# Kernel tuning notes

Hardware: AMD Instinct MI355X
Metric: run time of the kernel (lower is better)

The kernel has to match this reference:

```python
import jax, jax.numpy as jnp
import numpy as np

B = 65536      # batch
S = 256        # state_dim
A = 8          # n_agents
NA = 16        # n_actions
K = 10         # num_kernel
H = 64         # adv_hypernet_embed
AD = A * NA    # action_dim
D = S + AD     # state_dim + action_dim


def setup_inputs() -> dict:
    key = jax.random.key(0)
    ks = jax.random.split(key, 20)
    sc = 0.05
    inp = {
        'states': jax.random.normal(ks[0], (B, S), jnp.float32),
        'actions_onehot': jax.random.uniform(ks[1], (B, A, NA), jnp.float32),
        # key extractors: S -> H -> H -> 1, stacked over K kernels
        'kW1': jax.random.normal(ks[2], (K, H, S), jnp.float32) * sc,
        'kb1': jnp.zeros((K, H), jnp.float32),
        'kW2': jax.random.normal(ks[3], (K, H, H), jnp.float32) * sc,
        'kb2': jnp.zeros((K, H), jnp.float32),
        'kW3': jax.random.normal(ks[4], (K, 1, H), jnp.float32) * sc,
        'kb3': jnp.zeros((K, 1), jnp.float32),
        # agents extractors: S -> H -> H -> A
        'aW1': jax.random.normal(ks[5], (K, H, S), jnp.float32) * sc,
        'ab1': jnp.zeros((K, H), jnp.float32),
        'aW2': jax.random.normal(ks[6], (K, H, H), jnp.float32) * sc,
        'ab2': jnp.zeros((K, H), jnp.float32),
        'aW3': jax.random.normal(ks[7], (K, A, H), jnp.float32) * sc,
        'ab3': jnp.zeros((K, A), jnp.float32),
        # action extractors: S+AD -> H -> H -> A
        'cW1': jax.random.normal(ks[8], (K, H, D), jnp.float32) * sc,
        'cb1': jnp.zeros((K, H), jnp.float32),
        'cW2': jax.random.normal(ks[9], (K, H, H), jnp.float32) * sc,
        'cb2': jnp.zeros((K, H), jnp.float32),
        'cW3': jax.random.normal(ks[10], (K, A, H), jnp.float32) * sc,
        'cb3': jnp.zeros((K, A), jnp.float32),
    }
    return inp


def _mlp3(x, W1, b1, W2, b2, W3, b3):
    # x: [B, in] ; W1: [K, H, in] -> batched over K kernels in one GEMM
    h = jax.nn.relu(jnp.einsum('bd,khd->bkh', x, W1) + b1)        # [B,K,H]
    h = jax.nn.relu(jnp.einsum('bkh,kgh->bkg', h, W2) + b2)       # [B,K,H]
    return jnp.einsum('bkh,koh->bko', h, W3) + b3                 # [B,K,out]


def reference(states, actions_onehot,
              kW1, kb1, kW2, kb2, kW3, kb3,
              aW1, ab1, aW2, ab2, aW3, ab3,
              cW1, cb1, cW2, cb2, cW3, cb3):
    actions_flat = actions_onehot.reshape(states.shape[0], -1)    # [B, A*NA]
    data = jnp.concatenate([states, actions_flat], axis=1)        # [B, S+AD]

    x_key = jnp.abs(_mlp3(states, kW1, kb1, kW2, kb2, kW3, kb3)) + 1e-10   # [B,K,1]
    x_agents = jax.nn.sigmoid(_mlp3(states, aW1, ab1, aW2, ab2, aW3, ab3)) # [B,K,A]
    x_action = jax.nn.sigmoid(_mlp3(data, cW1, cb1, cW2, cb2, cW3, cb3))   # [B,K,A]

    # broadcast key over agents, multiply gates, sum over the K kernels
    head_attend = jnp.sum(x_key * x_agents * x_action, axis=1)    # [B,A]
    return head_attend
```

## Files before the change

### kernel.cpp

```cpp
#include <hip/hip_runtime.h>
#include <hip/hip_bf16.h>

#define Bsz 65536
#define Sdim 256
#define Aag 8
#define Kk 10
#define ADdim 128

#define SLAB_K_ELEMS 72704
#define NET_ELEMS 21504

typedef float f32x4 __attribute__((ext_vector_type(4)));
typedef __bf16 bf16x8 __attribute__((ext_vector_type(8)));

#define MFMA(a, b, cacc) __builtin_amdgcn_mfma_f32_16x16x32_bf16((a), (b), (cacc), 0, 0, 0)

__device__ __forceinline__ __bf16 f2bf(float f) {
    return (__bf16)f;
}

__device__ __forceinline__ unsigned int pack_bf2(float a, float b) {
    union { unsigned short s[2]; unsigned int u; } cv;
    union { unsigned short s; __bf16 b; } x;
    x.b = f2bf(a); cv.s[0] = x.s;
    x.b = f2bf(b); cv.s[1] = x.s;
    return cv.u;
}

__device__ __forceinline__ bf16x8 cvt8(float4 lo, float4 hi) {
    bf16x8 v;
    v[0] = f2bf(lo.x); v[1] = f2bf(lo.y); v[2] = f2bf(lo.z); v[3] = f2bf(lo.w);
    v[4] = f2bf(hi.x); v[5] = f2bf(hi.y); v[6] = f2bf(hi.z); v[7] = f2bf(hi.w);
    return v;
}

__device__ __forceinline__ int gperm(int n) {
    return ((n >> 5) << 5) + (((n >> 2) & 3) << 3) + (((n >> 4) & 1) << 2) + (n & 3);
}

__global__ void prep_weights(const float* __restrict__ kW1, const float* __restrict__ aW1,
                             const float* __restrict__ cW1, const float* __restrict__ kW2,
                             const float* __restrict__ aW2, const float* __restrict__ cW2,
                             const float* __restrict__ kW3, const float* __restrict__ aW3,
                             const float* __restrict__ cW3, __bf16* __restrict__ out) {
    int gid = blockIdx.x * 256 + threadIdx.x;
    if (gid >= 90880) return;
    int k = gid / 9088;
    int r = gid - k * 9088;
    int t, cn;
    if (r < 2688)      { t = 0; cn = r; }
    else if (r < 5376) { t = 1; cn = r - 2688; }
    else               { t = 2; cn = r - 5376; }
    const int KN = (t == 2) ? 384 : 256;
    const int CPR = KN / 8;
    const float* W1 = (t == 0) ? kW1 : (t == 1) ? aW1 : cW1;
    const float* W2 = (t == 0) ? kW2 : (t == 1) ? aW2 : cW2;
    const float* W3 = (t == 0) ? kW3 : (t == 1) ? aW3 : cW3;
    const int rows3 = (t == 0) ? 1 : 8;
    int dstchunk;
    const float* src = nullptr;
    if (cn < 64 * CPR) {
        int n = cn / CPR, k8 = cn - n * CPR;
        src = W1 + ((size_t)(k * 64 + gperm(n))) * KN + k8 * 8;
        dstchunk = n * CPR + (k8 ^ (n & 7));
    } else if (cn < 64 * CPR + 512) {
        int c2 = cn - 64 * CPR;
        int n = c2 >> 3, k8 = c2 & 7;
        src = W2 + ((size_t)(k * 64 + gperm(n))) * 64 + k8 * 8;
        dstchunk = 64 * CPR + n * 8 + (k8 ^ (n & 7));
    } else {
        int c3 = cn - 64 * CPR - 512;
        int n = c3 >> 3, k8 = c3 & 7;
        if (n < rows3) src = W3 + ((size_t)(k * rows3 + n)) * 64 + k8 * 8;
        dstchunk = 64 * CPR + 512 + n * 8 + (k8 ^ (n & 7));
    }
    bf16x8 v;
#pragma unroll
    for (int e = 0; e < 8; ++e) v[e] = src ? f2bf(src[e]) : (__bf16)0.0f;
    *(bf16x8*)(out + (size_t)k * SLAB_K_ELEMS + t * NET_ELEMS + dstchunk * 8) = v;
}

__device__ __forceinline__ void stage(const __bf16* __restrict__ src, __bf16* dst,
                                      int nchunks, int wave, int lane) {
    const char* g = (const char*)src + lane * 16;
    for (int ci = wave; ci < nchunks; ci += 8) {
        __builtin_amdgcn_global_load_lds(
            (const __attribute__((address_space(1))) void*)(g + ci * 1024),
            (__attribute__((address_space(3))) void*)((char*)dst + ci * 1024), 16, 0, 0);
    }
}

__device__ __forceinline__ bf16x8 frag_from_hp(const unsigned int (&hp)[4][2], int kb) {
    int4 u = {(int)hp[kb * 2][0], (int)hp[kb * 2][1], (int)hp[kb * 2 + 1][0], (int)hp[kb * 2 + 1][1]};
    return __builtin_bit_cast(bf16x8, u);
}

template <int KB, int MODE>
__device__ __forceinline__ void compute_net(
    const __bf16* __restrict__ W, const bf16x8 (&xf)[2][8],
    const float* __restrict__ actions, int rowbase,
    int q, int c, int k,
    const float* __restrict__ b1p, const float* __restrict__ b2p, const float* __restrict__ b3p,
    float (&keyv)[2], float (&ag)[2][4], float (&outacc)[2][4]) {
    constexpr int CPR = KB * 4;
    constexpr int W2O = 64 * CPR * 8;
    constexpr int W3O = W2O + 4096;

    bf16x8 xa[2][4];
    if (MODE == 2) {
#pragma unroll
        for (int s = 0; s < 2; ++s) {
            const float* ap = actions + (size_t)(rowbase + s * 16 + c) * ADdim + q * 8;
#pragma unroll
            for (int kb = 0; kb < 4; ++kb)
                xa[s][kb] = cvt8(*(const float4*)(ap + kb * 32), *(const float4*)(ap + kb * 32 + 4));
        }
    }

    f32x4 acc[4][2];
#pragma unroll
    for (int mt = 0; mt < 4; ++mt) {
        int base = ((mt >> 1) << 5) + (q << 3) + ((mt & 1) << 2);
        float4 bv = *(const float4*)(b1p + k * 64 + base);
        f32x4 b = {bv.x, bv.y, bv.z, bv.w};
        acc[mt][0] = b; acc[mt][1] = b;
    }
#pragma unroll
    for (int kb = 0; kb < KB; ++kb) {
        bf16x8 b0 = (kb < 8) ? xf[0][kb] : xa[0][kb - 8];
        bf16x8 b1 = (kb < 8) ? xf[1][kb] : xa[1][kb - 8];
#pragma unroll
        for (int mt = 0; mt < 4; ++mt) {
            int n = mt * 16 + c;
            bf16x8 a = *(const bf16x8*)(W + ((n * CPR + ((kb * 4 + q) ^ (n & 7))) << 3));
            acc[mt][0] = MFMA(a, b0, acc[mt][0]);
            acc[mt][1] = MFMA(a, b1, acc[mt][1]);
        }
    }
    unsigned int hp[2][4][2];
#pragma unroll
    for (int s = 0; s < 2; ++s)
#pragma unroll
        for (int mt = 0; mt < 4; ++mt) {
            hp[s][mt][0] = pack_bf2(fmaxf(acc[mt][s][0], 0.f), fmaxf(acc[mt][s][1], 0.f));
            hp[s][mt][1] = pack_bf2(fmaxf(acc[mt][s][2], 0.f), fmaxf(acc[mt][s][3], 0.f));
        }

    f32x4 acc2[4][2];
#pragma unroll
    for (int mt = 0; mt < 4; ++mt) {
        int base = ((mt >> 1) << 5) + (q << 3) + ((mt & 1) << 2);
        float4 bv = *(const float4*)(b2p + k * 64 + base);
        f32x4 b = {bv.x, bv.y, bv.z, bv.w};
        acc2[mt][0] = b; acc2[mt][1] = b;
    }
#pragma unroll
    for (int kb = 0; kb < 2; ++kb) {
        bf16x8 bh0 = frag_from_hp(hp[0], kb);
        bf16x8 bh1 = frag_from_hp(hp[1], kb);
#pragma unroll
        for (int mt = 0; mt < 4; ++mt) {
            int n = mt * 16 + c;
            bf16x8 a2 = *(const bf16x8*)(W + W2O + ((n * 8 + ((kb * 4 + q) ^ (n & 7))) << 3));
            acc2[mt][0] = MFMA(a2, bh0, acc2[mt][0]);
            acc2[mt][1] = MFMA(a2, bh1, acc2[mt][1]);
        }
    }
#pragma unroll
    for (int s = 0; s < 2; ++s)
#pragma unroll
        for (int mt = 0; mt < 4; ++mt) {
            hp[s][mt][0] = pack_bf2(fmaxf(acc2[mt][s][0], 0.f), fmaxf(acc2[mt][s][1], 0.f));
            hp[s][mt][1] = pack_bf2(fmaxf(acc2[mt][s][2], 0.f), fmaxf(acc2[mt][s][3], 0.f));
        }

    f32x4 acc3[2];
    if (MODE == 0) {
        float b3 = b3p[k];
        f32x4 z = {0.f, 0.f, 0.f, 0.f};
        if (q == 0) z[0] = b3;
        acc3[0] = z; acc3[1] = z;
    } else {
        f32x4 z = {0.f, 0.f, 0.f, 0.f};
        if (q < 2) {
            float4 bv = *(const float4*)(b3p + k * 8 + q * 4);
            z = {bv.x, bv.y, bv.z, bv.w};
        }
        acc3[0] = z; acc3[1] = z;
    }
#pragma unroll
    for (int kb = 0; kb < 2; ++kb) {
        bf16x8 a3 = *(const bf16x8*)(W + W3O + ((c * 8 + ((kb * 4 + q) ^ (c & 7))) << 3));
#pragma unroll
        for (int s = 0; s < 2; ++s) acc3[s] = MFMA(a3, frag_from_hp(hp[s], kb), acc3[s]);
    }
#pragma unroll
    for (int s = 0; s < 2; ++s) {
        if (MODE == 0) {
            float v = __shfl(acc3[s][0], c, 64);
            keyv[s] = fabsf(v) + 1e-10f;
        } else if (MODE == 1) {
#pragma unroll
            for (int i = 0; i < 4; ++i) ag[s][i] = 1.f / (1.f + __expf(-acc3[s][i]));
        } else {
#pragma unroll
            for (int i = 0; i < 4; ++i)
                outacc[s][i] += keyv[s] * ag[s][i] * (1.f / (1.f + __expf(-acc3[s][i])));
        }
    }
}

__global__ __launch_bounds__(512, 2) void qplex_main(
    const float* __restrict__ states, const float* __restrict__ actions,
    const __bf16* __restrict__ wbf,
    const float* __restrict__ b1k, const float* __restrict__ b2k, const float* __restrict__ b3k,
    const float* __restrict__ b1a, const float* __restrict__ b2a, const float* __restrict__ b3a,
    const float* __restrict__ b1c, const float* __restrict__ b2c, const float* __restrict__ b3c,
    float* __restrict__ out) {
    __shared__ __bf16 WB[2][29696];

    const int tid = threadIdx.x;
    const int lane = tid & 63;
    const int wave = tid >> 6;
    const int q = lane >> 4;
    const int c = lane & 15;
    const int rowbase = blockIdx.x * 256 + wave * 32;

    stage(wbf, WB[0], 42, wave, lane);

    bf16x8 xf[2][8];
#pragma unroll
    for (int s = 0; s < 2; ++s) {
        const float* srow = states + (size_t)(rowbase + s * 16 + c) * Sdim + q * 8;
#pragma unroll
        for (int kb = 0; kb < 8; ++kb)
            xf[s][kb] = cvt8(*(const float4*)(srow + kb * 32), *(const float4*)(srow + kb * 32 + 4));
    }

    float keyv[2];
    float ag[2][4];
    float outacc[2][4];
#pragma unroll
    for (int s = 0; s < 2; ++s) {
        keyv[s] = 0.f;
#pragma unroll
        for (int i = 0; i < 4; ++i) { ag[s][i] = 0.f; outacc[s][i] = 0.f; }
    }

    __syncthreads();

    for (int k = 0; k < Kk; ++k) {
        const __bf16* kslab = wbf + (size_t)k * SLAB_K_ELEMS;
        stage(kslab + NET_ELEMS, WB[(k + 1) & 1], 42, wave, lane);
        compute_net<8, 0>(&WB[k & 1][0], xf, actions, rowbase, q, c, k,
                          b1k, b2k, b3k, keyv, ag, outacc);
        __syncthreads();
        stage(kslab + 2 * NET_ELEMS, WB[k & 1], 58, wave, lane);
        compute_net<8, 1>(&WB[(k + 1) & 1][0], xf, actions, rowbase, q, c, k,
                          b1a, b2a, b3a, keyv, ag, outacc);
        __syncthreads();
        if (k < Kk - 1) stage(kslab + SLAB_K_ELEMS, WB[(k + 1) & 1], 42, wave, lane);
        compute_net<12, 2>(&WB[k & 1][0], xf, actions, rowbase, q, c, k,
                           b1c, b2c, b3c, keyv, ag, outacc);
        __syncthreads();
    }

    if (q < 2) {
#pragma unroll
        for (int s = 0; s < 2; ++s) {
            int r = rowbase + s * 16 + c;
            float4 v = {outacc[s][0], outacc[s][1], outacc[s][2], outacc[s][3]};
            *(float4*)(out + (size_t)r * Aag + q * 4) = v;
        }
    }
}

extern "C" void kernel_launch(void* const* d_in, const int* in_sizes, int n_in,
                              void* d_out, int out_size, void* d_ws, size_t ws_size,
                              hipStream_t stream) {
    const float* states = (const float*)d_in[0];
    const float* actions = (const float*)d_in[1];
    const float* kW1 = (const float*)d_in[2];
    const float* kb1 = (const float*)d_in[3];
    const float* kW2 = (const float*)d_in[4];
    const float* kb2 = (const float*)d_in[5];
    const float* kW3 = (const float*)d_in[6];
    const float* kb3 = (const float*)d_in[7];
    const float* aW1 = (const float*)d_in[8];
    const float* ab1 = (const float*)d_in[9];
    const float* aW2 = (const float*)d_in[10];
    const float* ab2 = (const float*)d_in[11];
    const float* aW3 = (const float*)d_in[12];
    const float* ab3 = (const float*)d_in[13];
    const float* cW1 = (const float*)d_in[14];
    const float* cb1 = (const float*)d_in[15];
    const float* cW2 = (const float*)d_in[16];
    const float* cb2 = (const float*)d_in[17];
    const float* cW3 = (const float*)d_in[18];
    const float* cb3 = (const float*)d_in[19];
    float* out = (float*)d_out;
    __bf16* wbf = (__bf16*)d_ws;

    prep_weights<<<355, 256, 0, stream>>>(kW1, aW1, cW1, kW2, aW2, cW2, kW3, aW3, cW3, wbf);
    qplex_main<<<256, 512, 0, stream>>>(states, actions, wbf, kb1, kb2, kb3,
                                        ab1, ab2, ab3, cb1, cb2, cb3, out);
}
```

Before: 278.7 us.

## Fuse key and agent MLPs per kernel and restage weights in two regions

The key and agents networks now run together in one fused pass. Both read the same state fragments, so their MFMA chains interleave and give more independent work per wave. Shared memory is restructured from two double-buffered net slots into one per-k slab: region A holds the key and agent weights and region B holds the action weights. This cuts the barriers per k-iteration from three to two. The cost is higher register pressure from the doubled accumulators and larger staging bursts per phase.

```diff
diff --git a/kernel.cpp b/kernel.cpp
--- a/kernel.cpp
+++ b/kernel.cpp
@@ -95,26 +95,141 @@
     return __builtin_bit_cast(bf16x8, u);
 }
 
-template <int KB, int MODE>
-__device__ __forceinline__ void compute_net(
+__device__ __forceinline__ void compute_fusedKA(
+    const __bf16* __restrict__ W, const bf16x8 (&xf)[2][8],
+    int q, int c, int k,
+    const float* __restrict__ b1k, const float* __restrict__ b2k, const float* __restrict__ b3k,
+    const float* __restrict__ b1a, const float* __restrict__ b2a, const float* __restrict__ b3a,
+    float (&keyv)[2], float (&ag)[2][4]) {
+    constexpr int CPR = 32;
+    constexpr int W2O = 64 * CPR * 8;
+    constexpr int W3O = W2O + 4096;
+    const __bf16* Wa = W + NET_ELEMS;
+
+    f32x4 accK[4][2], accA[4][2];
+#pragma unroll
+    for (int mt = 0; mt < 4; ++mt) {
+        int base = ((mt >> 1) << 5) + (q << 3) + ((mt & 1) << 2);
+        float4 bk = *(const float4*)(b1k + k * 64 + base);
+        float4 ba = *(const float4*)(b1a + k * 64 + base);
+        accK[mt][0] = {bk.x, bk.y, bk.z, bk.w}; accK[mt][1] = accK[mt][0];
+        accA[mt][0] = {ba.x, ba.y, ba.z, ba.w}; accA[mt][1] = accA[mt][0];
+    }
+#pragma unroll
+    for (int kb = 0; kb < 8; ++kb) {
+        bf16x8 b0 = xf[0][kb];
+        bf16x8 b1 = xf[1][kb];
+#pragma unroll
+        for (int mt = 0; mt < 4; ++mt) {
+            int n = mt * 16 + c;
+            int off = (n * CPR + ((kb * 4 + q) ^ (n & 7))) << 3;
+            bf16x8 aK = *(const bf16x8*)(W + off);
+            bf16x8 aA = *(const bf16x8*)(Wa + off);
+            accK[mt][0] = MFMA(aK, b0, accK[mt][0]);
+            accK[mt][1] = MFMA(aK, b1, accK[mt][1]);
+            accA[mt][0] = MFMA(aA, b0, accA[mt][0]);
+            accA[mt][1] = MFMA(aA, b1, accA[mt][1]);
+        }
+    }
+    unsigned int hpK[2][4][2], hpA[2][4][2];
+#pragma unroll
+    for (int s = 0; s < 2; ++s)
+#pragma unroll
+        for (int mt = 0; mt < 4; ++mt) {
+            hpK[s][mt][0] = pack_bf2(fmaxf(accK[mt][s][0], 0.f), fmaxf(accK[mt][s][1], 0.f));
+            hpK[s][mt][1] = pack_bf2(fmaxf(accK[mt][s][2], 0.f), fmaxf(accK[mt][s][3], 0.f));
+            hpA[s][mt][0] = pack_bf2(fmaxf(accA[mt][s][0], 0.f), fmaxf(accA[mt][s][1], 0.f));
+            hpA[s][mt][1] = pack_bf2(fmaxf(accA[mt][s][2], 0.f), fmaxf(accA[mt][s][3], 0.f));
+        }
+
+    f32x4 acc2K[4][2], acc2A[4][2];
+#pragma unroll
+    for (int mt = 0; mt < 4; ++mt) {
+        int base = ((mt >> 1) << 5) + (q << 3) + ((mt & 1) << 2);
+        float4 bk = *(const float4*)(b2k + k * 64 + base);
+        float4 ba = *(const float4*)(b2a + k * 64 + base);
+        acc2K[mt][0] = {bk.x, bk.y, bk.z, bk.w}; acc2K[mt][1] = acc2K[mt][0];
+        acc2A[mt][0] = {ba.x, ba.y, ba.z, ba.w}; acc2A[mt][1] = acc2A[mt][0];
+    }
+#pragma unroll
+    for (int kb = 0; kb < 2; ++kb) {
+        bf16x8 bhK0 = frag_from_hp(hpK[0], kb);
+        bf16x8 bhK1 = frag_from_hp(hpK[1], kb);
+        bf16x8 bhA0 = frag_from_hp(hpA[0], kb);
+        bf16x8 bhA1 = frag_from_hp(hpA[1], kb);
+#pragma unroll
+        for (int mt = 0; mt < 4; ++mt) {
+            int n = mt * 16 + c;
+            int off2 = W2O + ((n * 8 + ((kb * 4 + q) ^ (n & 7))) << 3);
+            bf16x8 a2K = *(const bf16x8*)(W + off2);
+            bf16x8 a2A = *(const bf16x8*)(Wa + off2);
+            acc2K[mt][0] = MFMA(a2K, bhK0, acc2K[mt][0]);
+            acc2K[mt][1] = MFMA(a2K, bhK1, acc2K[mt][1]);
+            acc2A[mt][0] = MFMA(a2A, bhA0, acc2A[mt][0]);
+            acc2A[mt][1] = MFMA(a2A, bhA1, acc2A[mt][1]);
+        }
+    }
+#pragma unroll
+    for (int s = 0; s < 2; ++s)
+#pragma unroll
+        for (int mt = 0; mt < 4; ++mt) {
+            hpK[s][mt][0] = pack_bf2(fmaxf(acc2K[mt][s][0], 0.f), fmaxf(acc2K[mt][s][1], 0.f));
+            hpK[s][mt][1] = pack_bf2(fmaxf(acc2K[mt][s][2], 0.f), fmaxf(acc2K[mt][s][3], 0.f));
+            hpA[s][mt][0] = pack_bf2(fmaxf(acc2A[mt][s][0], 0.f), fmaxf(acc2A[mt][s][1], 0.f));
+            hpA[s][mt][1] = pack_bf2(fmaxf(acc2A[mt][s][2], 0.f), fmaxf(acc2A[mt][s][3], 0.f));
+        }
+
+    f32x4 accK3[2], accA3[2];
+    {
+        float b3 = b3k[k];
+        f32x4 zk = {0.f, 0.f, 0.f, 0.f};
+        if (q == 0) zk[0] = b3;
+        accK3[0] = zk; accK3[1] = zk;
+        f32x4 za = {0.f, 0.f, 0.f, 0.f};
+        if (q < 2) {
+            float4 bv = *(const float4*)(b3a + k * 8 + q * 4);
+            za = {bv.x, bv.y, bv.z, bv.w};
+        }
+        accA3[0] = za; accA3[1] = za;
+    }
+#pragma unroll
+    for (int kb = 0; kb < 2; ++kb) {
+        int off3 = W3O + ((c * 8 + ((kb * 4 + q) ^ (c & 7))) << 3);
+        bf16x8 a3K = *(const bf16x8*)(W + off3);
+        bf16x8 a3A = *(const bf16x8*)(Wa + off3);
+#pragma unroll
+        for (int s = 0; s < 2; ++s) {
+            accK3[s] = MFMA(a3K, frag_from_hp(hpK[s], kb), accK3[s]);
+            accA3[s] = MFMA(a3A, frag_from_hp(hpA[s], kb), accA3[s]);
+        }
+    }
+#pragma unroll
+    for (int s = 0; s < 2; ++s) {
+        float v = __shfl(accK3[s][0], c, 64);
+        keyv[s] = fabsf(v) + 1e-10f;
+#pragma unroll
+        for (int i = 0; i < 4; ++i) ag[s][i] = 1.f / (1.f + __expf(-accA3[s][i]));
+    }
+}
+
+__device__ __forceinline__ void compute_action(
     const __bf16* __restrict__ W, const bf16x8 (&xf)[2][8],
     const float* __restrict__ actions, int rowbase,
     int q, int c, int k,
     const float* __restrict__ b1p, const float* __restrict__ b2p, const float* __restrict__ b3p,
-    float (&keyv)[2], float (&ag)[2][4], float (&outacc)[2][4]) {
+    const float (&keyv)[2], const float (&ag)[2][4], float (&outacc)[2][4]) {
+    constexpr int KB = 12;
     constexpr int CPR = KB * 4;
     constexpr int W2O = 64 * CPR * 8;
     constexpr int W3O = W2O + 4096;
 
     bf16x8 xa[2][4];
-    if (MODE == 2) {
-#pragma unroll
-        for (int s = 0; s < 2; ++s) {
-            const float* ap = actions + (size_t)(rowbase + s * 16 + c) * ADdim + q * 8;
-#pragma unroll
-            for (int kb = 0; kb < 4; ++kb)
-                xa[s][kb] = cvt8(*(const float4*)(ap + kb * 32), *(const float4*)(ap + kb * 32 + 4));
-        }
+#pragma unroll
+    for (int s = 0; s < 2; ++s) {
+        const float* ap = actions + (size_t)(rowbase + s * 16 + c) * ADdim + q * 8;
+#pragma unroll
+        for (int kb = 0; kb < 4; ++kb)
+            xa[s][kb] = cvt8(*(const float4*)(ap + kb * 32), *(const float4*)(ap + kb * 32 + 4));
     }
 
     f32x4 acc[4][2];
@@ -122,8 +237,7 @@
     for (int mt = 0; mt < 4; ++mt) {
         int base = ((mt >> 1) << 5) + (q << 3) + ((mt & 1) << 2);
         float4 bv = *(const float4*)(b1p + k * 64 + base);
-        f32x4 b = {bv.x, bv.y, bv.z, bv.w};
-        acc[mt][0] = b; acc[mt][1] = b;
+        acc[mt][0] = {bv.x, bv.y, bv.z, bv.w}; acc[mt][1] = acc[mt][0];
     }
 #pragma unroll
     for (int kb = 0; kb < KB; ++kb) {
@@ -151,8 +265,7 @@
     for (int mt = 0; mt < 4; ++mt) {
         int base = ((mt >> 1) << 5) + (q << 3) + ((mt & 1) << 2);
         float4 bv = *(const float4*)(b2p + k * 64 + base);
-        f32x4 b = {bv.x, bv.y, bv.z, bv.w};
-        acc2[mt][0] = b; acc2[mt][1] = b;
+        acc2[mt][0] = {bv.x, bv.y, bv.z, bv.w}; acc2[mt][1] = acc2[mt][0];
     }
 #pragma unroll
     for (int kb = 0; kb < 2; ++kb) {
@@ -175,12 +288,7 @@
         }
 
     f32x4 acc3[2];
-    if (MODE == 0) {
-        float b3 = b3p[k];
-        f32x4 z = {0.f, 0.f, 0.f, 0.f};
-        if (q == 0) z[0] = b3;
-        acc3[0] = z; acc3[1] = z;
-    } else {
+    {
         f32x4 z = {0.f, 0.f, 0.f, 0.f};
         if (q < 2) {
             float4 bv = *(const float4*)(b3p + k * 8 + q * 4);
@@ -195,19 +303,10 @@
         for (int s = 0; s < 2; ++s) acc3[s] = MFMA(a3, frag_from_hp(hp[s], kb), acc3[s]);
     }
 #pragma unroll
-    for (int s = 0; s < 2; ++s) {
-        if (MODE == 0) {
-            float v = __shfl(acc3[s][0], c, 64);
-            keyv[s] = fabsf(v) + 1e-10f;
-        } else if (MODE == 1) {
-#pragma unroll
-            for (int i = 0; i < 4; ++i) ag[s][i] = 1.f / (1.f + __expf(-acc3[s][i]));
-        } else {
-#pragma unroll
-            for (int i = 0; i < 4; ++i)
-                outacc[s][i] += keyv[s] * ag[s][i] * (1.f / (1.f + __expf(-acc3[s][i])));
-        }
-    }
+    for (int s = 0; s < 2; ++s)
+#pragma unroll
+        for (int i = 0; i < 4; ++i)
+            outacc[s][i] += keyv[s] * ag[s][i] * (1.f / (1.f + __expf(-acc3[s][i])));
 }
 
 __global__ __launch_bounds__(512, 2) void qplex_main(
@@ -217,7 +316,9 @@
     const float* __restrict__ b1a, const float* __restrict__ b2a, const float* __restrict__ b3a,
     const float* __restrict__ b1c, const float* __restrict__ b2c, const float* __restrict__ b3c,
     float* __restrict__ out) {
-    __shared__ __bf16 WB[2][29696];
+    __shared__ __bf16 WB[SLAB_K_ELEMS];
+    __bf16* RA = WB;
+    __bf16* RB = WB + 2 * NET_ELEMS;
 
     const int tid = threadIdx.x;
     const int lane = tid & 63;
@@ -226,7 +327,7 @@
     const int c = lane & 15;
     const int rowbase = blockIdx.x * 256 + wave * 32;
 
-    stage(wbf, WB[0], 42, wave, lane);
+    stage(wbf, RA, 84, wave, lane);
 
     bf16x8 xf[2][8];
 #pragma unroll
@@ -251,17 +352,11 @@
 
     for (int k = 0; k < Kk; ++k) {
         const __bf16* kslab = wbf + (size_t)k * SLAB_K_ELEMS;
-        stage(kslab + NET_ELEMS, WB[(k + 1) & 1], 42, wave, lane);
-        compute_net<8, 0>(&WB[k & 1][0], xf, actions, rowbase, q, c, k,
-                          b1k, b2k, b3k, keyv, ag, outacc);
+        stage(kslab + 2 * NET_ELEMS, RB, 58, wave, lane);
+        compute_fusedKA(RA, xf, q, c, k, b1k, b2k, b3k, b1a, b2a, b3a, keyv, ag);
         __syncthreads();
-        stage(kslab + 2 * NET_ELEMS, WB[k & 1], 58, wave, lane);
-        compute_net<8, 1>(&WB[(k + 1) & 1][0], xf, actions, rowbase, q, c, k,
-                          b1a, b2a, b3a, keyv, ag, outacc);
-        __syncthreads();
-        if (k < Kk - 1) stage(kslab + SLAB_K_ELEMS, WB[(k + 1) & 1], 42, wave, lane);
-        compute_net<12, 2>(&WB[k & 1][0], xf, actions, rowbase, q, c, k,
-                           b1c, b2c, b3c, keyv, ag, outacc);
+        if (k < Kk - 1) stage(kslab + SLAB_K_ELEMS, RA, 84, wave, lane);
+        compute_action(RB, xf, actions, rowbase, q, c, k, b1c, b2c, b3c, keyv, ag, outacc);
         __syncthreads();
     }
 
```

After: 390.1 us. 40.0% more time.

## Read MFMA weight fragments directly from global memory instead of staging through LDS

Applied to the files above, without the earlier changes.

Removes the double-buffered LDS staging of the per-kernel weight slabs and the block-wide barriers. Each lane now loads its bf16 weight fragments straight from the global workspace, relying on L1/L2 caching. To make those loads coalesced, the prep layout becomes k8-major. Each wave now handles 16 rows instead of 32, launched as 1024 blocks of 256 threads, which trades weight reuse per load for fewer registers and higher occupancy.

```diff
diff --git a/kernel.cpp b/kernel.cpp
--- a/kernel.cpp
+++ b/kernel.cpp
@@ -62,32 +62,22 @@
     if (cn < 64 * CPR) {
         int n = cn / CPR, k8 = cn - n * CPR;
         src = W1 + ((size_t)(k * 64 + gperm(n))) * KN + k8 * 8;
-        dstchunk = n * CPR + (k8 ^ (n & 7));
+        dstchunk = k8 * 64 + n;
     } else if (cn < 64 * CPR + 512) {
         int c2 = cn - 64 * CPR;
         int n = c2 >> 3, k8 = c2 & 7;
         src = W2 + ((size_t)(k * 64 + gperm(n))) * 64 + k8 * 8;
-        dstchunk = 64 * CPR + n * 8 + (k8 ^ (n & 7));
+        dstchunk = 64 * CPR + k8 * 64 + n;
     } else {
         int c3 = cn - 64 * CPR - 512;
         int n = c3 >> 3, k8 = c3 & 7;
         if (n < rows3) src = W3 + ((size_t)(k * rows3 + n)) * 64 + k8 * 8;
-        dstchunk = 64 * CPR + 512 + n * 8 + (k8 ^ (n & 7));
+        dstchunk = 64 * CPR + 512 + k8 * 16 + n;
     }
     bf16x8 v;
 #pragma unroll
     for (int e = 0; e < 8; ++e) v[e] = src ? f2bf(src[e]) : (__bf16)0.0f;
     *(bf16x8*)(out + (size_t)k * SLAB_K_ELEMS + t * NET_ELEMS + dstchunk * 8) = v;
-}
-
-__device__ __forceinline__ void stage(const __bf16* __restrict__ src, __bf16* dst,
-                                      int nchunks, int wave, int lane) {
-    const char* g = (const char*)src + lane * 16;
-    for (int ci = wave; ci < nchunks; ci += 8) {
-        __builtin_amdgcn_global_load_lds(
-            (const __attribute__((address_space(1))) void*)(g + ci * 1024),
-            (__attribute__((address_space(3))) void*)((char*)dst + ci * 1024), 16, 0, 0);
-    }
 }
 
 __device__ __forceinline__ bf16x8 frag_from_hp(const unsigned int (&hp)[4][2], int kb) {
@@ -97,181 +87,135 @@
 
 template <int KB, int MODE>
 __device__ __forceinline__ void compute_net(
-    const __bf16* __restrict__ W, const bf16x8 (&xf)[2][8],
-    const float* __restrict__ actions, int rowbase,
+    const __bf16* __restrict__ W, const bf16x8 (&xf)[8], const bf16x8 (&xa)[4],
     int q, int c, int k,
     const float* __restrict__ b1p, const float* __restrict__ b2p, const float* __restrict__ b3p,
-    float (&keyv)[2], float (&ag)[2][4], float (&outacc)[2][4]) {
+    float& keyv, float (&ag)[4], float (&outacc)[4]) {
     constexpr int CPR = KB * 4;
     constexpr int W2O = 64 * CPR * 8;
     constexpr int W3O = W2O + 4096;
 
-    bf16x8 xa[2][4];
-    if (MODE == 2) {
-#pragma unroll
-        for (int s = 0; s < 2; ++s) {
-            const float* ap = actions + (size_t)(rowbase + s * 16 + c) * ADdim + q * 8;
-#pragma unroll
-            for (int kb = 0; kb < 4; ++kb)
-                xa[s][kb] = cvt8(*(const float4*)(ap + kb * 32), *(const float4*)(ap + kb * 32 + 4));
-        }
-    }
-
-    f32x4 acc[4][2];
+    f32x4 acc[4];
 #pragma unroll
     for (int mt = 0; mt < 4; ++mt) {
         int base = ((mt >> 1) << 5) + (q << 3) + ((mt & 1) << 2);
         float4 bv = *(const float4*)(b1p + k * 64 + base);
-        f32x4 b = {bv.x, bv.y, bv.z, bv.w};
-        acc[mt][0] = b; acc[mt][1] = b;
+        acc[mt] = {bv.x, bv.y, bv.z, bv.w};
     }
 #pragma unroll
     for (int kb = 0; kb < KB; ++kb) {
-        bf16x8 b0 = (kb < 8) ? xf[0][kb] : xa[0][kb - 8];
-        bf16x8 b1 = (kb < 8) ? xf[1][kb] : xa[1][kb - 8];
+        bf16x8 b = (kb < 8) ? xf[kb] : xa[kb - 8];
 #pragma unroll
         for (int mt = 0; mt < 4; ++mt) {
-            int n = mt * 16 + c;
-            bf16x8 a = *(const bf16x8*)(W + ((n * CPR + ((kb * 4 + q) ^ (n & 7))) << 3));
-            acc[mt][0] = MFMA(a, b0, acc[mt][0]);
-            acc[mt][1] = MFMA(a, b1, acc[mt][1]);
+            bf16x8 a = *(const bf16x8*)(W + ((kb * 256 + q * 64 + mt * 16 + c) << 3));
+            acc[mt] = MFMA(a, b, acc[mt]);
         }
     }
-    unsigned int hp[2][4][2];
-#pragma unroll
-    for (int s = 0; s < 2; ++s)
-#pragma unroll
-        for (int mt = 0; mt < 4; ++mt) {
-            hp[s][mt][0] = pack_bf2(fmaxf(acc[mt][s][0], 0.f), fmaxf(acc[mt][s][1], 0.f));
-            hp[s][mt][1] = pack_bf2(fmaxf(acc[mt][s][2], 0.f), fmaxf(acc[mt][s][3], 0.f));
-        }
-
-    f32x4 acc2[4][2];
+    unsigned int hp[4][2];
+#pragma unroll
+    for (int mt = 0; mt < 4; ++mt) {
+        hp[mt][0] = pack_bf2(fmaxf(acc[mt][0], 0.f), fmaxf(acc[mt][1], 0.f));
+        hp[mt][1] = pack_bf2(fmaxf(acc[mt][2], 0.f), fmaxf(acc[mt][3], 0.f));
+    }
+
+    f32x4 acc2[4];
 #pragma unroll
     for (int mt = 0; mt < 4; ++mt) {
         int base = ((mt >> 1) << 5) + (q << 3) + ((mt & 1) << 2);
         float4 bv = *(const float4*)(b2p + k * 64 + base);
-        f32x4 b = {bv.x, bv.y, bv.z, bv.w};
-        acc2[mt][0] = b; acc2[mt][1] = b;
+        acc2[mt] = {bv.x, bv.y, bv.z, bv.w};
     }
 #pragma unroll
     for (int kb = 0; kb < 2; ++kb) {
-        bf16x8 bh0 = frag_from_hp(hp[0], kb);
-        bf16x8 bh1 = frag_from_hp(hp[1], kb);
+        bf16x8 bh = frag_from_hp(hp, kb);
 #pragma unroll
         for (int mt = 0; mt < 4; ++mt) {
-            int n = mt * 16 + c;
-            bf16x8 a2 = *(const bf16x8*)(W + W2O + ((n * 8 + ((kb * 4 + q) ^ (n & 7))) << 3));
-            acc2[mt][0] = MFMA(a2, bh0, acc2[mt][0]);
-            acc2[mt][1] = MFMA(a2, bh1, acc2[mt][1]);
+            bf16x8 a2 = *(const bf16x8*)(W + W2O + ((kb * 256 + q * 64 + mt * 16 + c) << 3));
+            acc2[mt] = MFMA(a2, bh, acc2[mt]);
         }
     }
 #pragma unroll
-    for (int s = 0; s < 2; ++s)
-#pragma unroll
-        for (int mt = 0; mt < 4; ++mt) {
-            hp[s][mt][0] = pack_bf2(fmaxf(acc2[mt][s][0], 0.f), fmaxf(acc2[mt][s][1], 0.f));
-            hp[s][mt][1] = pack_bf2(fmaxf(acc2[mt][s][2], 0.f), fmaxf(acc2[mt][s][3], 0.f));
-        }
-
-    f32x4 acc3[2];
+    for (int mt = 0; mt < 4; ++mt) {
+        hp[mt][0] = pack_bf2(fmaxf(acc2[mt][0], 0.f), fmaxf(acc2[mt][1], 0.f));
+        hp[mt][1] = pack_bf2(fmaxf(acc2[mt][2], 0.f), fmaxf(acc2[mt][3], 0.f));
+    }
+
+    f32x4 acc3;
     if (MODE == 0) {
         float b3 = b3p[k];
         f32x4 z = {0.f, 0.f, 0.f, 0.f};
         if (q == 0) z[0] = b3;
-        acc3[0] = z; acc3[1] = z;
+        acc3 = z;
     } else {
         f32x4 z = {0.f, 0.f, 0.f, 0.f};
         if (q < 2) {
             float4 bv = *(const float4*)(b3p + k * 8 + q * 4);
             z = {bv.x, bv.y, bv.z, bv.w};
         }
-        acc3[0] = z; acc3[1] = z;
+        acc3 = z;
     }
 #pragma unroll
     for (int kb = 0; kb < 2; ++kb) {
-        bf16x8 a3 = *(const bf16x8*)(W + W3O + ((c * 8 + ((kb * 4 + q) ^ (c & 7))) << 3));
-#pragma unroll
-        for (int s = 0; s < 2; ++s) acc3[s] = MFMA(a3, frag_from_hp(hp[s], kb), acc3[s]);
-    }
-#pragma unroll
-    for (int s = 0; s < 2; ++s) {
-        if (MODE == 0) {
-            float v = __shfl(acc3[s][0], c, 64);
-            keyv[s] = fabsf(v) + 1e-10f;
-        } else if (MODE == 1) {
-#pragma unroll
-            for (int i = 0; i < 4; ++i) ag[s][i] = 1.f / (1.f + __expf(-acc3[s][i]));
-        } else {
-#pragma unroll
-            for (int i = 0; i < 4; ++i)
-                outacc[s][i] += keyv[s] * ag[s][i] * (1.f / (1.f + __expf(-acc3[s][i])));
-        }
-    }
-}
-
-__global__ __launch_bounds__(512, 2) void qplex_main(
+        bf16x8 a3 = *(const bf16x8*)(W + W3O + ((kb * 64 + q * 16 + c) << 3));
+        acc3 = MFMA(a3, frag_from_hp(hp, kb), acc3);
+    }
+    if (MODE == 0) {
+        float v = __shfl(acc3[0], c, 64);
+        keyv = fabsf(v) + 1e-10f;
+    } else if (MODE == 1) {
+#pragma unroll
+        for (int i = 0; i < 4; ++i) ag[i] = 1.f / (1.f + __expf(-acc3[i]));
+    } else {
+#pragma unroll
+        for (int i = 0; i < 4; ++i)
+            outacc[i] += keyv * ag[i] * (1.f / (1.f + __expf(-acc3[i])));
+    }
+}
+
+__global__ __launch_bounds__(256, 4) void qplex_main(
     const float* __restrict__ states, const float* __restrict__ actions,
     const __bf16* __restrict__ wbf,
     const float* __restrict__ b1k, const float* __restrict__ b2k, const float* __restrict__ b3k,
     const float* __restrict__ b1a, const float* __restrict__ b2a, const float* __restrict__ b3a,
     const float* __restrict__ b1c, const float* __restrict__ b2c, const float* __restrict__ b3c,
     float* __restrict__ out) {
-    __shared__ __bf16 WB[2][29696];
-
     const int tid = threadIdx.x;
     const int lane = tid & 63;
     const int wave = tid >> 6;
     const int q = lane >> 4;
     const int c = lane & 15;
-    const int rowbase = blockIdx.x * 256 + wave * 32;
-
-    stage(wbf, WB[0], 42, wave, lane);
-
-    bf16x8 xf[2][8];
-#pragma unroll
-    for (int s = 0; s < 2; ++s) {
-        const float* srow = states + (size_t)(rowbase + s * 16 + c) * Sdim + q * 8;
+    const int row = blockIdx.x * 64 + wave * 16 + c;
+
+    bf16x8 xf[8];
+    {
+        const float* srow = states + (size_t)row * Sdim + q * 8;
 #pragma unroll
         for (int kb = 0; kb < 8; ++kb)
-            xf[s][kb] = cvt8(*(const float4*)(srow + kb * 32), *(const float4*)(srow + kb * 32 + 4));
-    }
-
-    float keyv[2];
-    float ag[2][4];
-    float outacc[2][4];
-#pragma unroll
-    for (int s = 0; s < 2; ++s) {
-        keyv[s] = 0.f;
-#pragma unroll
-        for (int i = 0; i < 4; ++i) { ag[s][i] = 0.f; outacc[s][i] = 0.f; }
-    }
-
-    __syncthreads();
-
+            xf[kb] = cvt8(*(const float4*)(srow + kb * 32), *(const float4*)(srow + kb * 32 + 4));
+    }
+    bf16x8 xa[4];
+    {
+        const float* arow = actions + (size_t)row * ADdim + q * 8;
+#pragma unroll
+        for (int kb = 0; kb < 4; ++kb)
+            xa[kb] = cvt8(*(const float4*)(arow + kb * 32), *(const float4*)(arow + kb * 32 + 4));
+    }
+
+    float keyv = 0.f;
+    float ag[4] = {0.f, 0.f, 0.f, 0.f};
+    float outacc[4] = {0.f, 0.f, 0.f, 0.f};
+
+#pragma unroll 1
     for (int k = 0; k < Kk; ++k) {
         const __bf16* kslab = wbf + (size_t)k * SLAB_K_ELEMS;
-        stage(kslab + NET_ELEMS, WB[(k + 1) & 1], 42, wave, lane);
-        compute_net<8, 0>(&WB[k & 1][0], xf, actions, rowbase, q, c, k,
-                          b1k, b2k, b3k, keyv, ag, outacc);
-        __syncthreads();
-        stage(kslab + 2 * NET_ELEMS, WB[k & 1], 58, wave, lane);
-        compute_net<8, 1>(&WB[(k + 1) & 1][0], xf, actions, rowbase, q, c, k,
-                          b1a, b2a, b3a, keyv, ag, outacc);
-        __syncthreads();
-        if (k < Kk - 1) stage(kslab + SLAB_K_ELEMS, WB[(k + 1) & 1], 42, wave, lane);
-        compute_net<12, 2>(&WB[k & 1][0], xf, actions, rowbase, q, c, k,
-                           b1c, b2c, b3c, keyv, ag, outacc);
-        __syncthreads();
+        compute_net<8, 0>(kslab, xf, xa, q, c, k, b1k, b2k, b3k, keyv, ag, outacc);
+        compute_net<8, 1>(kslab + NET_ELEMS, xf, xa, q, c, k, b1a, b2a, b3a, keyv, ag, outacc);
+        compute_net<12, 2>(kslab + 2 * NET_ELEMS, xf, xa, q, c, k, b1c, b2c, b3c, keyv, ag, outacc);
     }
 
     if (q < 2) {
-#pragma unroll
-        for (int s = 0; s < 2; ++s) {
-            int r = rowbase + s * 16 + c;
-            float4 v = {outacc[s][0], outacc[s][1], outacc[s][2], outacc[s][3]};
-            *(float4*)(out + (size_t)r * Aag + q * 4) = v;
-        }
+        float4 v = {outacc[0], outacc[1], outacc[2], outacc[3]};
+        *(float4*)(out + (size_t)row * Aag + q * 4) = v;
     }
 }
 
@@ -302,6 +246,6 @@
     __bf16* wbf = (__bf16*)d_ws;
 
     prep_weights<<<355, 256, 0, stream>>>(kW1, aW1, cW1, kW2, aW2, cW2, kW3, aW3, cW3, wbf);
-    qplex_main<<<256, 512, 0, stream>>>(states, actions, wbf, kb1, kb2, kb3,
-                                        ab1, ab2, ab3, cb1, cb2, cb3, out);
-}
+    qplex_main<<<1024, 256, 0, stream>>>(states, actions, wbf, kb1, kb2, kb3,
+                                         ab1, ab2, ab3, cb1, cb2, cb3, out);
+}
```

Measured after the change: 551.9 us. 1.98x slower.
